# Optimization experiments

Measured on AMD Instinct MI355X. Metric: run time of the kernel, lower is better.

The kernel has to match this reference:

```python
import jax, jax.numpy as jnp
import numpy as np

BSZ, MAX_LEN, D, D_ATTN = 256, 1024, 256, 128

def setup_inputs() -> dict:
    key = jax.random.key(0)
    k1, k2, k3, k4, k5 = jax.random.split(key, 5)
    # xavier-uniform-like scales for params
    s_wf = float(np.sqrt(6.0 / (D_ATTN + D)))
    s_bf = float(np.sqrt(6.0 / (D + D_ATTN)))
    s_wh = float(np.sqrt(6.0 / (D_ATTN + 1)))
    return {
        "emb_q": jax.random.normal(k1, (BSZ, D), dtype=jnp.float32),
        "emb_iseq": jax.random.normal(k2, (BSZ, MAX_LEN, D), dtype=jnp.float32),
        "w_f": jax.random.uniform(k3, (D, D_ATTN, D), dtype=jnp.float32, minval=-s_wf, maxval=s_wf),
        "b_f": jax.random.uniform(k4, (D, D_ATTN), dtype=jnp.float32, minval=-s_bf, maxval=s_bf),
        "w_h": jax.random.uniform(k5, (D_ATTN, 1), dtype=jnp.float32, minval=-s_wh, maxval=s_wh),
    }

def reference(emb_q, emb_iseq, w_f, b_f, w_h):
    # trans_q[b, j, a] = sum_k w_f[j, a, k] * emb_q[b, k]   -> [bsz, d, d_attn]
    trans_q = jnp.einsum("jak,bk->bja", w_f, emb_q)
    h_q_att = jnp.tanh(trans_q + b_f[None, :, :])            # [bsz, d, d_attn]
    # h_iq[b, l, a] = sum_j emb_iseq[b, l, j] * h_q_att[b, j, a]
    # weight[b, l] = sum_a h_iq[b, l, a] * w_h[a, 0]
    weight_attn = jnp.einsum("blj,bja,a->bl", emb_iseq, h_q_att, w_h[:, 0])
    return weight_attn
```

## Files before the change

### kernel.cpp

```cpp
#include <hip/hip_runtime.h>
#include <hip/hip_bf16.h>
#include <math.h>

#define BSZ 256
#define MAX_LEN 1024
#define DD 256
#define DA 128

typedef short short8 __attribute__((ext_vector_type(8)));
typedef short short4v __attribute__((ext_vector_type(4)));
typedef float floatx4 __attribute__((ext_vector_type(4)));

__device__ __forceinline__ short f2bf(float f) {
    union { float f; unsigned u; } x;
    x.f = f;
    unsigned r = (x.u + 0x7FFFu + ((x.u >> 16) & 1u)) >> 16;
    return (short)r;
}

__global__ __launch_bounds__(256, 1) void v_kernel(
    const float* __restrict__ emb_q,
    const float* __restrict__ w_f,
    const float* __restrict__ b_f,
    const float* __restrict__ w_h,
    float* __restrict__ v)
{
    __shared__ short lds_b[DA * DD];
    const int j   = blockIdx.x;
    const int tid = threadIdx.x;

    const float* wj = w_f + (size_t)j * (DA * DD);
    #pragma unroll
    for (int it = 0; it < 32; ++it) {
        int f4 = tid + it * 256;
        int a  = f4 >> 6;
        int kq = f4 & 63;
        float4 val = ((const float4*)wj)[f4];
        int c    = kq >> 1;
        int half = kq & 1;
        int sc   = c ^ (a & 31);
        short4v s;
        s[0] = f2bf(val.x); s[1] = f2bf(val.y); s[2] = f2bf(val.z); s[3] = f2bf(val.w);
        *(short4v*)&lds_b[a * DD + sc * 8 + half * 4] = s;
    }
    __syncthreads();

    const int lane = tid & 63;
    const int wave = tid >> 6;
    const int l15  = lane & 15;
    const int quad = lane >> 4;

    short8 afrag[4][8];
    #pragma unroll
    for (int t = 0; t < 4; ++t) {
        const int b0 = (wave * 4 + t) * 16;
        const float* arow = emb_q + (size_t)(b0 + l15) * DD + quad * 8;
        #pragma unroll
        for (int ks = 0; ks < 8; ++ks) {
            float4 v0 = ((const float4*)(arow + ks * 32))[0];
            float4 v1 = ((const float4*)(arow + ks * 32))[1];
            short8 f;
            f[0]=f2bf(v0.x); f[1]=f2bf(v0.y); f[2]=f2bf(v0.z); f[3]=f2bf(v0.w);
            f[4]=f2bf(v1.x); f[5]=f2bf(v1.y); f[6]=f2bf(v1.z); f[7]=f2bf(v1.w);
            afrag[t][ks] = f;
        }
    }

    float p[4][4];
    #pragma unroll
    for (int t = 0; t < 4; ++t) { p[t][0]=0.f; p[t][1]=0.f; p[t][2]=0.f; p[t][3]=0.f; }

    for (int at = 0; at < 8; ++at) {
        const int a0  = at * 16;
        const int a   = a0 + l15;
        const float bfv = b_f[j * DA + a];
        const float whv = w_h[a];
        floatx4 acc[4];
        #pragma unroll
        for (int t = 0; t < 4; ++t) acc[t] = (floatx4){0.f, 0.f, 0.f, 0.f};
        #pragma unroll
        for (int ks = 0; ks < 8; ++ks) {
            const int sc = (4 * ks + quad) ^ (a & 31);
            short8 bfrag = *(const short8*)&lds_b[a * DD + sc * 8];
            #pragma unroll
            for (int t = 0; t < 4; ++t)
                acc[t] = __builtin_amdgcn_mfma_f32_16x16x32_bf16(afrag[t][ks], bfrag, acc[t], 0, 0, 0);
        }
        #pragma unroll
        for (int t = 0; t < 4; ++t)
            #pragma unroll
            for (int r = 0; r < 4; ++r)
                p[t][r] += tanhf(acc[t][r] + bfv) * whv;
    }

    #pragma unroll
    for (int t = 0; t < 4; ++t) {
        #pragma unroll
        for (int r = 0; r < 4; ++r) {
            float s = p[t][r];
            s += __shfl_xor(s, 1);
            s += __shfl_xor(s, 2);
            s += __shfl_xor(s, 4);
            s += __shfl_xor(s, 8);
            if (l15 == 0) {
                const int b = (wave * 4 + t) * 16 + quad * 4 + r;
                v[b * DD + j] = s;
            }
        }
    }
}

__global__ __launch_bounds__(256, 8) void w_kernel(
    const float* __restrict__ emb_iseq,
    const float* __restrict__ v,
    float* __restrict__ out)
{
    const int tid  = threadIdx.x;
    const int lane = tid & 63;
    const int wave = tid >> 6;
    const int b    = blockIdx.x >> 3;
    const int lc   = blockIdx.x & 7;

    const float4 vv = ((const float4*)(v + b * DD))[lane];
    const float* base = emb_iseq + ((size_t)b * MAX_LEN + (size_t)lc * 128) * DD;
    float* obase = out + b * MAX_LEN + lc * 128;

    #pragma unroll 4
    for (int it = 0; it < 32; ++it) {
        const int l = wave * 32 + it;
        float4 e = ((const float4*)(base + (size_t)l * DD))[lane];
        float s = e.x * vv.x + e.y * vv.y + e.z * vv.z + e.w * vv.w;
        s += __shfl_xor(s, 32);
        s += __shfl_xor(s, 16);
        s += __shfl_xor(s, 8);
        s += __shfl_xor(s, 4);
        s += __shfl_xor(s, 2);
        s += __shfl_xor(s, 1);
        if (lane == 0) obase[l] = s;
    }
}

extern "C" void kernel_launch(void* const* d_in, const int* in_sizes, int n_in,
                              void* d_out, int out_size, void* d_ws, size_t ws_size,
                              hipStream_t stream) {
    const float* emb_q    = (const float*)d_in[0];
    const float* emb_iseq = (const float*)d_in[1];
    const float* w_f      = (const float*)d_in[2];
    const float* b_f      = (const float*)d_in[3];
    const float* w_h      = (const float*)d_in[4];
    float* out = (float*)d_out;
    float* v   = (float*)d_ws;

    v_kernel<<<256, 256, 0, stream>>>(emb_q, w_f, b_f, w_h, v);
    w_kernel<<<2048, 256, 0, stream>>>(emb_iseq, v, out);
}
```

Baseline: 404.4 us.

## Double-buffer w_f staging, use fast exp2-based tanh, nontemporal emb_iseq loads

The v_kernel now stages w_f into LDS in two halves. The second half's global loads are issued while the first half is being computed with MFMA, so load latency overlaps compute. tanhf is replaced with an exp2/rcp approximation to cut transcendental cost, at some accuracy risk near saturation. The streaming emb_iseq reads in w_kernel use nontemporal loads to reduce cache pollution.

```diff
diff --git a/kernel.cpp b/kernel.cpp
--- a/kernel.cpp
+++ b/kernel.cpp
@@ -16,6 +16,25 @@
     x.f = f;
     unsigned r = (x.u + 0x7FFFu + ((x.u >> 16) & 1u)) >> 16;
     return (short)r;
+}
+
+__device__ __forceinline__ float fast_exp2(float x) {
+#if __has_builtin(__builtin_amdgcn_exp2f)
+    return __builtin_amdgcn_exp2f(x);
+#else
+    return exp2f(x);
+#endif
+}
+__device__ __forceinline__ float fast_rcp(float x) {
+#if __has_builtin(__builtin_amdgcn_rcpf)
+    return __builtin_amdgcn_rcpf(x);
+#else
+    return 1.0f / x;
+#endif
+}
+__device__ __forceinline__ float fast_tanh(float x) {
+    float e = fast_exp2(x * 2.8853900817779268f);
+    return 1.0f - 2.0f * fast_rcp(e + 1.0f);
 }
 
 __global__ __launch_bounds__(256, 1) void v_kernel(
@@ -25,25 +44,15 @@
     const float* __restrict__ w_h,
     float* __restrict__ v)
 {
-    __shared__ short lds_b[DA * DD];
+    __shared__ short lds_b[2][64 * DD];
     const int j   = blockIdx.x;
     const int tid = threadIdx.x;
-
     const float* wj = w_f + (size_t)j * (DA * DD);
-    #pragma unroll
-    for (int it = 0; it < 32; ++it) {
-        int f4 = tid + it * 256;
-        int a  = f4 >> 6;
-        int kq = f4 & 63;
-        float4 val = ((const float4*)wj)[f4];
-        int c    = kq >> 1;
-        int half = kq & 1;
-        int sc   = c ^ (a & 31);
-        short4v s;
-        s[0] = f2bf(val.x); s[1] = f2bf(val.y); s[2] = f2bf(val.z); s[3] = f2bf(val.w);
-        *(short4v*)&lds_b[a * DD + sc * 8 + half * 4] = s;
-    }
-    __syncthreads();
+
+    float4 tmp[16];
+    #pragma unroll
+    for (int it = 0; it < 16; ++it)
+        tmp[it] = ((const float4*)wj)[tid + it * 256];
 
     const int lane = tid & 63;
     const int wave = tid >> 6;
@@ -66,13 +75,32 @@
         }
     }
 
+    #pragma unroll
+    for (int it = 0; it < 16; ++it) {
+        int f4 = tid + it * 256;
+        int al = f4 >> 6;
+        int kq = f4 & 63;
+        int c    = kq >> 1;
+        int hf   = kq & 1;
+        int sc   = c ^ (al & 31);
+        short4v s;
+        s[0] = f2bf(tmp[it].x); s[1] = f2bf(tmp[it].y);
+        s[2] = f2bf(tmp[it].z); s[3] = f2bf(tmp[it].w);
+        *(short4v*)&lds_b[0][al * DD + sc * 8 + hf * 4] = s;
+    }
+    __syncthreads();
+
+    #pragma unroll
+    for (int it = 0; it < 16; ++it)
+        tmp[it] = ((const float4*)(wj + 64 * DD))[tid + it * 256];
+
     float p[4][4];
     #pragma unroll
     for (int t = 0; t < 4; ++t) { p[t][0]=0.f; p[t][1]=0.f; p[t][2]=0.f; p[t][3]=0.f; }
 
-    for (int at = 0; at < 8; ++at) {
-        const int a0  = at * 16;
-        const int a   = a0 + l15;
+    auto computeAt = [&](int at, int h) {
+        const int a   = at * 16 + l15;
+        const int al  = a & 63;
         const float bfv = b_f[j * DA + a];
         const float whv = w_h[a];
         floatx4 acc[4];
@@ -80,8 +108,8 @@
         for (int t = 0; t < 4; ++t) acc[t] = (floatx4){0.f, 0.f, 0.f, 0.f};
         #pragma unroll
         for (int ks = 0; ks < 8; ++ks) {
-            const int sc = (4 * ks + quad) ^ (a & 31);
-            short8 bfrag = *(const short8*)&lds_b[a * DD + sc * 8];
+            const int sc = (4 * ks + quad) ^ (al & 31);
+            short8 bfrag = *(const short8*)&lds_b[h][al * DD + sc * 8];
             #pragma unroll
             for (int t = 0; t < 4; ++t)
                 acc[t] = __builtin_amdgcn_mfma_f32_16x16x32_bf16(afrag[t][ks], bfrag, acc[t], 0, 0, 0);
@@ -90,8 +118,29 @@
         for (int t = 0; t < 4; ++t)
             #pragma unroll
             for (int r = 0; r < 4; ++r)
-                p[t][r] += tanhf(acc[t][r] + bfv) * whv;
-    }
+                p[t][r] += fast_tanh(acc[t][r] + bfv) * whv;
+    };
+
+    #pragma unroll
+    for (int at = 0; at < 4; ++at) computeAt(at, 0);
+
+    #pragma unroll
+    for (int it = 0; it < 16; ++it) {
+        int f4 = tid + it * 256;
+        int al = f4 >> 6;
+        int kq = f4 & 63;
+        int c    = kq >> 1;
+        int hf   = kq & 1;
+        int sc   = c ^ (al & 31);
+        short4v s;
+        s[0] = f2bf(tmp[it].x); s[1] = f2bf(tmp[it].y);
+        s[2] = f2bf(tmp[it].z); s[3] = f2bf(tmp[it].w);
+        *(short4v*)&lds_b[1][al * DD + sc * 8 + hf * 4] = s;
+    }
+    __syncthreads();
+
+    #pragma unroll
+    for (int at = 4; at < 8; ++at) computeAt(at, 1);
 
     #pragma unroll
     for (int t = 0; t < 4; ++t) {
@@ -121,15 +170,15 @@
     const int b    = blockIdx.x >> 3;
     const int lc   = blockIdx.x & 7;
 
-    const float4 vv = ((const float4*)(v + b * DD))[lane];
+    const floatx4 vv = ((const floatx4*)(v + b * DD))[lane];
     const float* base = emb_iseq + ((size_t)b * MAX_LEN + (size_t)lc * 128) * DD;
     float* obase = out + b * MAX_LEN + lc * 128;
 
     #pragma unroll 4
     for (int it = 0; it < 32; ++it) {
         const int l = wave * 32 + it;
-        float4 e = ((const float4*)(base + (size_t)l * DD))[lane];
-        float s = e.x * vv.x + e.y * vv.y + e.z * vv.z + e.w * vv.w;
+        floatx4 e = __builtin_nontemporal_load((const floatx4*)(base + (size_t)l * DD) + lane);
+        float s = e[0] * vv[0] + e[1] * vv[1] + e[2] * vv[2] + e[3] * vv[3];
         s += __shfl_xor(s, 32);
         s += __shfl_xor(s, 16);
         s += __shfl_xor(s, 8);
```

After: 379.7 us (median of 2 runs). -6.1%, faster.
